# Performance work log

Measured on AMD Instinct MI355X. Metric: run time of the kernel, lower is better.

The kernel has to match this reference:

```python
import jax, jax.numpy as jnp
import numpy as np

K = 3
PAD = 1


def conv3x3(x, w, b):
    # x: [B,Ci,H,W], w: [Co,Ci,3,3] -> [B,Co,H,W]
    y = jax.lax.conv_general_dilated(
        x, w, window_strides=(1, 1), padding=((PAD, PAD), (PAD, PAD)),
        dimension_numbers=('NCHW', 'OIHW', 'NCHW'))
    return y + b[None, :, None, None]


def _gather(x_flat, idx):
    # x_flat: [C, H*W], idx: [K2*H*W] -> [C, K2*H*W]
    return x_flat[:, idx]


def deform_sample(x, off_x, off_y, mask):
    """Modulated deformable im2col (DCNv2, dg=1, stride=1, pad=1, dil=1).
    x: [B,C,H,W]; off_x, off_y, mask: [B,K2,H,W] -> cols [B,C,K2,H,W]."""
    B, C, H, W = x.shape
    K2 = K * K
    # static kernel-tap displacements relative to output pixel
    dy = jnp.repeat(jnp.arange(K), K) - PAD          # [K2]
    dx = jnp.tile(jnp.arange(K), K) - PAD            # [K2]
    gy = jnp.arange(H)[:, None].astype(x.dtype)      # [H,1]
    gx = jnp.arange(W)[None, :].astype(x.dtype)      # [1,W]
    ys = gy[None, None] + dy[None, :, None, None].astype(x.dtype) + off_y  # [B,K2,H,W]
    xs = gx[None, None] + dx[None, :, None, None].astype(x.dtype) + off_x
    y0 = jnp.floor(ys)
    x0 = jnp.floor(xs)
    wy1 = ys - y0
    wx1 = xs - x0
    xf = x.reshape(B, C, H * W)
    val = jnp.zeros((B, C, K2, H, W), x.dtype)
    for oy, ox in ((0, 0), (0, 1), (1, 0), (1, 1)):
        yy = y0 + oy
        xx = x0 + ox
        wgt = (wy1 if oy else 1.0 - wy1) * (wx1 if ox else 1.0 - wx1)
        valid = ((yy >= 0) & (yy < H) & (xx >= 0) & (xx < W)).astype(x.dtype)
        idx = (jnp.clip(yy, 0, H - 1) * W + jnp.clip(xx, 0, W - 1)).astype(jnp.int32)
        g = jax.vmap(_gather)(xf, idx.reshape(B, -1)).reshape(B, C, K2, H, W)
        val = val + (wgt * valid)[:, None] * g
    return val * mask[:, None]  # modulation, broadcast over C


def reference(x, feat, w_off, b_off, w_def, b_def):
    # offset/mask prediction conv (3*K2 channels), chunked as in the torch module
    om = conv3x3(feat, w_off, b_off)
    off_x, off_y, m = jnp.split(om, 3, axis=1)   # each [B,K2,H,W]
    mask = jax.nn.sigmoid(m)
    cols = deform_sample(x, off_x, off_y, mask)  # [B,C,K2,H,W]
    O = w_def.shape[0]
    out = jnp.einsum('bckhw,ock->bohw', cols, w_def.reshape(O, -1, K * K))
    out = out + b_def[None, :, None, None]
    return jax.nn.relu(out)


def setup_inputs() -> dict:
    key = jax.random.key(0)
    k1, k2, k3, k4 = jax.random.split(key, 4)
    B, C, O, H, W = 4, 64, 64, 128, 128
    K2 = K * K
    x = jax.random.normal(k1, (B, C, H, W), jnp.float32)
    feat = jax.random.normal(k2, (B, C, H, W), jnp.float32)
    # offset conv params: small init so offsets stay near zero (as in practice)
    w_off = jax.random.normal(k3, (3 * K2, C, 3, 3), jnp.float32) * 0.01
    b_off = jnp.zeros((3 * K2,), jnp.float32)
    w_def = jax.random.normal(k4, (O, C, 3, 3), jnp.float32) * (1.0 / np.sqrt(C * K2))
    b_def = jnp.zeros((O,), jnp.float32)
    return {"x": x, "feat": feat, "w_off": w_off, "b_off": b_off,
            "w_def": w_def, "b_def": b_def}
```

## Files before the change

### kernel.cpp

```cpp
#include <hip/hip_runtime.h>
#include <math.h>

#define Bn 4
#define Cn 64
#define On 64
#define Hn 128
#define Wn 128
#define HWn (Hn * Wn)

typedef __attribute__((ext_vector_type(8))) short s16x8;
typedef __attribute__((ext_vector_type(4))) float f32x4;

__device__ __forceinline__ unsigned short f2bf(float f) {
    unsigned u = __float_as_uint(f);
    u += 0x7fffu + ((u >> 16) & 1u);
    return (unsigned short)(u >> 16);
}
__device__ __forceinline__ float bf2f(unsigned short u) {
    return __uint_as_float(((unsigned)u) << 16);
}
__device__ __forceinline__ int swz(int row, int ch) {
    return row * 32 + (((ch ^ (row >> 1)) & 3) << 3);
}

__global__ __launch_bounds__(256) void transpose_all(const float* __restrict__ x,
                                                     const float* __restrict__ feat,
                                                     const float* __restrict__ wdef,
                                                     const float* __restrict__ woff,
                                                     ushort* __restrict__ xt,
                                                     ushort* __restrict__ ft,
                                                     ushort* __restrict__ wdT2,
                                                     ushort* __restrict__ woT2) {
    int t = threadIdx.x;
    if (blockIdx.z == 2) {
        int id = (blockIdx.y * gridDim.x + blockIdx.x) * 256 + t;
        if (id < 36864) {
            int c2 = id & 31, oc = (id >> 5) & 63, ks = id >> 11;
            int k = ks % 9, s = ks / 9;
            wdT2[id] = f2bf(wdef[(oc * 64 + s * 32 + c2) * 9 + k]);
        } else if (id < 55296) {
            int i2 = id - 36864;
            int c2 = i2 & 31, oc = (i2 >> 5) & 31, ks = i2 >> 10;
            int k = ks % 9, s = ks / 9;
            woT2[i2] = (oc < 27) ? f2bf(woff[(oc * 64 + s * 32 + c2) * 9 + k]) : (ushort)0;
        }
        return;
    }
    __shared__ float tile[64][65];
    const float* src = blockIdx.z ? feat : x;
    ushort* dst0 = blockIdx.z ? ft : xt;
    int b = blockIdx.y, hw0 = blockIdx.x * 64;
    int lane = t & 63, grp = t >> 6;
    const float* xb = src + (size_t)b * Cn * HWn;
#pragma unroll
    for (int i = 0; i < 16; ++i) {
        int c = grp * 16 + i;
        tile[lane][c] = xb[(size_t)c * HWn + hw0 + lane];
    }
    __syncthreads();
#pragma unroll
    for (int jj = 0; jj < 2; ++jj) {
        int px = jj * 32 + (t >> 3), ch = t & 7;
        s16x8 p;
#pragma unroll
        for (int j = 0; j < 8; ++j) p[j] = (short)f2bf(tile[px][ch * 8 + j]);
        *(s16x8*)(dst0 + ((size_t)(b * HWn + hw0 + px)) * Cn + ch * 8) = p;
    }
}

__global__ __launch_bounds__(256, 3) void off_conv_kernel(const ushort* __restrict__ ft,
                                                          const ushort* __restrict__ woT2,
                                                          const float* __restrict__ b_off,
                                                          float* __restrict__ om) {
    __shared__ __align__(16) char smem[43776];
    ushort* s_win = (ushort*)smem;
    ushort* s_wgt = (ushort*)(smem + 25344);
    float* s_out = (float*)smem;

    int t = threadIdx.x;
    int wv = t >> 6, l = t & 63;
    int q = l >> 4, r = l & 15;
    int h = blockIdx.x, b = blockIdx.y;
    const ushort* ft_b = ft + (size_t)b * HWn * Cn;

    f32x4 zero = {0.f, 0.f, 0.f, 0.f};
    s16x8 zz = {0, 0, 0, 0, 0, 0, 0, 0};
    f32x4 acc[2][2];
    acc[0][0] = zero; acc[0][1] = zero; acc[1][0] = zero; acc[1][1] = zero;

    for (int s = 0; s < 2; ++s) {
        for (int j = t; j < 1560; j += 256) {
            int row = j / 520, rm = j - row * 520;
            int col = rm >> 2, ch = rm & 3;
            int rs = min(max(h - 1 + row, 0), Hn - 1);
            int cs = min(max(col - 1, 0), Wn - 1);
            s16x8 v = *(const s16x8*)(ft_b + (size_t)(rs * Wn + cs) * Cn + s * 32 + ch * 8);
            *(s16x8*)&s_win[swz(row * 132 + col, ch)] = v;
        }
        for (int j = t; j < 1152; j += 256) {
            int ro = j >> 2, ch = j & 3;
            s16x8 v = *(const s16x8*)(woT2 + (size_t)s * 9216 + ro * 32 + ch * 8);
            *(s16x8*)&s_wgt[swz(ro, ch)] = v;
        }
        __syncthreads();
#pragma unroll 3
        for (int k = 0; k < 9; ++k) {
            int dy = k / 3 - 1, dx = k % 3 - 1;
            int y = h + dy;
            bool yv = (y >= 0) && (y < Hn);
#pragma unroll
            for (int mt = 0; mt < 2; ++mt) {
                int px = wv * 32 + mt * 16 + r;
                int xx = px + dx;
                bool valid = yv && (xx >= 0) && (xx < Wn);
                int lin = (dy + 1) * 132 + px + dx + 1;
                s16x8 av = *(const s16x8*)&s_win[swz(lin, q)];
                av = valid ? av : zz;
#pragma unroll
                for (int ot = 0; ot < 2; ++ot) {
                    s16x8 bv = *(const s16x8*)&s_wgt[swz(k * 32 + ot * 16 + r, q)];
                    acc[mt][ot] = __builtin_amdgcn_mfma_f32_16x16x32_bf16(av, bv, acc[mt][ot], 0, 0, 0);
                }
            }
        }
        __syncthreads();
    }
#pragma unroll
    for (int mt = 0; mt < 2; ++mt)
#pragma unroll
        for (int ot = 0; ot < 2; ++ot) {
            int oc = ot * 16 + r;
            float bo = (oc < 27) ? b_off[oc] : 0.f;
#pragma unroll
            for (int reg = 0; reg < 4; ++reg) {
                int px = wv * 32 + mt * 16 + q * 4 + reg;
                float v = acc[mt][ot][reg] + bo;
                if (oc >= 18 && oc < 27) v = 1.f / (1.f + __expf(-v));
                s_out[oc * 132 + px] = v;
            }
        }
    __syncthreads();
    for (int idx = t; idx < 27 * 128; idx += 256) {
        int o = idx >> 7, px = idx & 127;
        om[((size_t)b * 27 + o) * HWn + h * Wn + px] = s_out[o * 132 + px];
    }
}

__global__ __launch_bounds__(256, 3) void mega_kernel(const ushort* __restrict__ xt,
                                                      const ushort* __restrict__ wdT2,
                                                      const float* __restrict__ om,
                                                      const float* __restrict__ b_def,
                                                      float* __restrict__ out) {
    __shared__ __align__(16) char smem[24576];
    ushort* s_win = (ushort*)smem;
    float* s_out = (float*)smem;

    int t = threadIdx.x;
    int wv = t >> 6, l = t & 63;
    int q = l >> 4, r = l & 15;
    int blk = (blockIdx.x & 7) * 256 + (blockIdx.x >> 3);
    int p0 = blk * 32;
    int b = p0 >> 14;
    int rem = p0 & (HWn - 1);
    int h = rem >> 7;
    int wbase = rem & (Wn - 1);
    int pxh = wv & 1, och = wv >> 1;
    int pxi = pxh * 16 + r;
    float pxif = (float)pxi;
    const ushort* xt_b = xt + (size_t)b * HWn * Cn;

#pragma unroll
    for (int i = 0; i < 6; ++i) {
        int jb = i * 256 + wv * 64;
        int j = jb + l;
        int lin = j >> 3, slot = j & 7;
        int linc = min(lin, 179);
        int cidx = (slot - lin) & 7;
        int row = linc / 36, col = linc - row * 36;
        int rs = min(max(h - 2 + row, 0), Hn - 1);
        int cs = min(max(wbase - 2 + col, 0), Wn - 1);
        const ushort* gp = xt_b + (size_t)(rs * Wn + cs) * Cn + cidx * 8;
        __builtin_amdgcn_global_load_lds(
            (const __attribute__((address_space(1))) unsigned int*)gp,
            (__attribute__((address_space(3))) unsigned int*)(s_win + (size_t)jb * 8),
            16, 0, 0);
    }

    const float* om_b = om + ((size_t)b * 27) * HWn + h * Wn + wbase + pxi;
    float omv[27];
#pragma unroll
    for (int o = 0; o < 27; ++o) omv[o] = om_b[(size_t)o * HWn];

    bool okp = true;
#pragma unroll
    for (int k = 0; k < 9; ++k) {
        float uy = (float)(k / 3 - 1) + omv[9 + k];
        float ux = pxif + (float)(k % 3 - 1) + omv[k];
        okp = okp && (uy >= -2.f) && (uy < 2.f) && (ux >= -2.f) && (ux < 33.f);
    }
    int fast = __all(okp) ? 1 : 0;

    __syncthreads();

    f32x4 zero = {0.f, 0.f, 0.f, 0.f};
    f32x4 acc[2];
    acc[0] = zero; acc[1] = zero;

    if (fast) {
#pragma unroll 3
        for (int k = 0; k < 9; ++k) {
            float uy = (float)(k / 3 - 1) + omv[9 + k];
            float ux = pxif + (float)(k % 3 - 1) + omv[k];
            float mv = omv[18 + k];
            float y0f = floorf(uy), x0f = floorf(ux);
            float fy = uy - y0f, fx = ux - x0f;
            int iy = (int)y0f + 2;
            int ix = (int)x0f + 2;
            int yab = h + (int)y0f, xab = wbase + (int)x0f;
            bool vy0 = (yab >= 0) && (yab < Hn);
            bool vy1 = (yab + 1 >= 0) && (yab + 1 < Hn);
            bool vx0 = (xab >= 0) && (xab < Wn);
            bool vx1 = (xab + 1 >= 0) && (xab + 1 < Wn);
            float g0 = (vy0 && vx0) ? (1.f - fy) * (1.f - fx) * mv : 0.f;
            float g1 = (vy0 && vx1) ? (1.f - fy) * fx * mv : 0.f;
            float g2 = (vy1 && vx0) ? fy * (1.f - fx) * mv : 0.f;
            float g3 = (vy1 && vx1) ? fy * fx * mv : 0.f;
            int l0 = iy * 36 + ix, l1 = l0 + 1, l2 = l0 + 36, l3 = l0 + 37;
            s16x8 bw[2][2];
#pragma unroll
            for (int s = 0; s < 2; ++s)
#pragma unroll
                for (int ot = 0; ot < 2; ++ot)
                    bw[s][ot] = *(const s16x8*)(wdT2 + (size_t)s * 18432
                                                + (size_t)(k * 64 + och * 32 + ot * 16 + r) * 32 + q * 8);
            s16x8 af[2];
#pragma unroll
            for (int s = 0; s < 2; ++s) {
                int c = s * 4 + q;
                s16x8 q0 = *(const s16x8*)&s_win[l0 * 64 + (((c + l0) & 7) << 3)];
                s16x8 q1 = *(const s16x8*)&s_win[l1 * 64 + (((c + l1) & 7) << 3)];
                s16x8 q2 = *(const s16x8*)&s_win[l2 * 64 + (((c + l2) & 7) << 3)];
                s16x8 q3 = *(const s16x8*)&s_win[l3 * 64 + (((c + l3) & 7) << 3)];
                s16x8 p;
#pragma unroll
                for (int j = 0; j < 8; ++j) {
                    float rr = g0 * bf2f((unsigned short)q0[j]) + g1 * bf2f((unsigned short)q1[j])
                             + g2 * bf2f((unsigned short)q2[j]) + g3 * bf2f((unsigned short)q3[j]);
                    p[j] = (short)f2bf(rr);
                }
                af[s] = p;
            }
#pragma unroll
            for (int s = 0; s < 2; ++s)
#pragma unroll
                for (int ot = 0; ot < 2; ++ot)
                    acc[ot] = __builtin_amdgcn_mfma_f32_16x16x32_bf16(af[s], bw[s][ot], acc[ot], 0, 0, 0);
        }
    } else {
#pragma unroll 1
        for (int k = 0; k < 9; ++k) {
            float ys = (float)(h + k / 3 - 1) + omv[9 + k];
            float xs = (float)(wbase + pxi + k % 3 - 1) + omv[k];
            float mv = omv[18 + k];
            float y0f = floorf(ys), x0f = floorf(xs);
            float fy = ys - y0f, fx = xs - x0f;
            int y0 = (int)y0f, x0 = (int)x0f;
            float g[4];
            int a[4];
#pragma unroll
            for (int n = 0; n < 4; ++n) {
                int yy = y0 + (n >> 1), xx = x0 + (n & 1);
                bool valid = (yy >= 0) && (yy < Hn) && (xx >= 0) && (xx < Wn);
                float wgt = ((n >> 1) ? fy : 1.f - fy) * ((n & 1) ? fx : 1.f - fx) * mv;
                g[n] = valid ? wgt : 0.f;
                int yc = min(max(yy, 0), Hn - 1), xc = min(max(xx, 0), Wn - 1);
                a[n] = (yc * Wn + xc) * Cn;
            }
#pragma unroll
            for (int s = 0; s < 2; ++s) {
                int c = s * 32 + q * 8;
                s16x8 q0 = *(const s16x8*)(xt_b + a[0] + c);
                s16x8 q1 = *(const s16x8*)(xt_b + a[1] + c);
                s16x8 q2 = *(const s16x8*)(xt_b + a[2] + c);
                s16x8 q3 = *(const s16x8*)(xt_b + a[3] + c);
                s16x8 af;
#pragma unroll
                for (int j = 0; j < 8; ++j) {
                    float rr = g[0] * bf2f((unsigned short)q0[j]) + g[1] * bf2f((unsigned short)q1[j])
                             + g[2] * bf2f((unsigned short)q2[j]) + g[3] * bf2f((unsigned short)q3[j]);
                    af[j] = (short)f2bf(rr);
                }
#pragma unroll
                for (int ot = 0; ot < 2; ++ot) {
                    s16x8 bv = *(const s16x8*)(wdT2 + (size_t)s * 18432
                                               + (size_t)(k * 64 + och * 32 + ot * 16 + r) * 32 + q * 8);
                    acc[ot] = __builtin_amdgcn_mfma_f32_16x16x32_bf16(af, bv, acc[ot], 0, 0, 0);
                }
            }
        }
    }
    __syncthreads();

#pragma unroll
    for (int ot = 0; ot < 2; ++ot) {
        int oc = och * 32 + ot * 16 + r;
        float bv = b_def[oc];
        f32x4 vv;
#pragma unroll
        for (int reg = 0; reg < 4; ++reg) vv[reg] = fmaxf(acc[ot][reg] + bv, 0.f);
        *(f32x4*)&s_out[oc * 34 + pxh * 16 + q * 4] = vv;
    }
    __syncthreads();
    {
        int px = t & 31, og = t >> 5;
        float* ob = out + ((size_t)b * On) * HWn + h * Wn + wbase;
#pragma unroll
        for (int j = 0; j < 8; ++j) {
            int oc = og * 8 + j;
            ob[(size_t)oc * HWn + px] = s_out[oc * 34 + px];
        }
    }
}

extern "C" void kernel_launch(void* const* d_in, const int* in_sizes, int n_in,
                              void* d_out, int out_size, void* d_ws, size_t ws_size,
                              hipStream_t stream) {
    const float* x = (const float*)d_in[0];
    const float* feat = (const float*)d_in[1];
    const float* w_off = (const float*)d_in[2];
    const float* b_off = (const float*)d_in[3];
    const float* w_def = (const float*)d_in[4];
    const float* b_def = (const float*)d_in[5];
    float* out = (float*)d_out;

    char* ws = (char*)d_ws;
    ushort* xt = (ushort*)ws;
    ushort* ft = (ushort*)(ws + 8388608);
    ushort* wdT2 = (ushort*)(ws + 16777216);
    ushort* woT2 = (ushort*)(ws + 16850944);
    float* om = (float*)(ws + 16887808);

    hipLaunchKernelGGL(transpose_all, dim3(HWn / 64, Bn, 3), dim3(256), 0, stream,
                       x, feat, w_def, w_off, xt, ft, wdT2, woT2);
    hipLaunchKernelGGL(off_conv_kernel, dim3(Hn, Bn), dim3(256), 0, stream,
                       ft, woT2, b_off, om);
    hipLaunchKernelGGL(mega_kernel, dim3((Bn * HWn) / 32), dim3(256), 0, stream,
                       xt, wdT2, om, b_def, out);
}
```

Measured before the change: 141.0 us.

## Split offset conv per half-row and widen deform tile to 2x32 pixels

The offset-conv kernel now processes half a row (64 pixels) per block, which doubles the grid and shrinks its LDS footprint. This should raise occupancy and parallelism. The deform mega kernel now covers a 2-row by 32-pixel tile, with each wave computing all 64 output channels instead of half. This reuses the staged 5-row input window across two rows and halves the number of blocks, in exchange for more accumulator registers, more weight loads per wave, and slightly more LDS.

After: 128.3 us. 9.0% less time.

```diff
diff --git a/kernel.cpp b/kernel.cpp
--- a/kernel.cpp
+++ b/kernel.cpp
@@ -72,30 +72,31 @@
                                                           const ushort* __restrict__ woT2,
                                                           const float* __restrict__ b_off,
                                                           float* __restrict__ om) {
-    __shared__ __align__(16) char smem[43776];
+    __shared__ __align__(16) char smem[31488];
     ushort* s_win = (ushort*)smem;
-    ushort* s_wgt = (ushort*)(smem + 25344);
+    ushort* s_wgt = (ushort*)(smem + 13056);
     float* s_out = (float*)smem;
 
     int t = threadIdx.x;
     int wv = t >> 6, l = t & 63;
     int q = l >> 4, r = l & 15;
-    int h = blockIdx.x, b = blockIdx.y;
+    int h = blockIdx.x >> 1, wb = (blockIdx.x & 1) * 64;
+    int b = blockIdx.y;
     const ushort* ft_b = ft + (size_t)b * HWn * Cn;
 
     f32x4 zero = {0.f, 0.f, 0.f, 0.f};
     s16x8 zz = {0, 0, 0, 0, 0, 0, 0, 0};
-    f32x4 acc[2][2];
-    acc[0][0] = zero; acc[0][1] = zero; acc[1][0] = zero; acc[1][1] = zero;
+    f32x4 acc[2];
+    acc[0] = zero; acc[1] = zero;
 
     for (int s = 0; s < 2; ++s) {
-        for (int j = t; j < 1560; j += 256) {
-            int row = j / 520, rm = j - row * 520;
+        for (int j = t; j < 816; j += 256) {
+            int row = j / 272, rm = j - row * 272;
             int col = rm >> 2, ch = rm & 3;
             int rs = min(max(h - 1 + row, 0), Hn - 1);
-            int cs = min(max(col - 1, 0), Wn - 1);
+            int cs = min(max(wb - 1 + col, 0), Wn - 1);
             s16x8 v = *(const s16x8*)(ft_b + (size_t)(rs * Wn + cs) * Cn + s * 32 + ch * 8);
-            *(s16x8*)&s_win[swz(row * 132 + col, ch)] = v;
+            *(s16x8*)&s_win[swz(row * 68 + col, ch)] = v;
         }
         for (int j = t; j < 1152; j += 256) {
             int ro = j >> 2, ch = j & 3;
@@ -108,41 +109,36 @@
             int dy = k / 3 - 1, dx = k % 3 - 1;
             int y = h + dy;
             bool yv = (y >= 0) && (y < Hn);
-#pragma unroll
-            for (int mt = 0; mt < 2; ++mt) {
-                int px = wv * 32 + mt * 16 + r;
-                int xx = px + dx;
-                bool valid = yv && (xx >= 0) && (xx < Wn);
-                int lin = (dy + 1) * 132 + px + dx + 1;
-                s16x8 av = *(const s16x8*)&s_win[swz(lin, q)];
-                av = valid ? av : zz;
-#pragma unroll
-                for (int ot = 0; ot < 2; ++ot) {
-                    s16x8 bv = *(const s16x8*)&s_wgt[swz(k * 32 + ot * 16 + r, q)];
-                    acc[mt][ot] = __builtin_amdgcn_mfma_f32_16x16x32_bf16(av, bv, acc[mt][ot], 0, 0, 0);
-                }
+            int px = wv * 16 + r;
+            int xx = wb + px + dx;
+            bool valid = yv && (xx >= 0) && (xx < Wn);
+            int lin = (dy + 1) * 68 + px + dx + 1;
+            s16x8 av = *(const s16x8*)&s_win[swz(lin, q)];
+            av = valid ? av : zz;
+#pragma unroll
+            for (int ot = 0; ot < 2; ++ot) {
+                s16x8 bv = *(const s16x8*)&s_wgt[swz(k * 32 + ot * 16 + r, q)];
+                acc[ot] = __builtin_amdgcn_mfma_f32_16x16x32_bf16(av, bv, acc[ot], 0, 0, 0);
             }
         }
         __syncthreads();
     }
 #pragma unroll
-    for (int mt = 0; mt < 2; ++mt)
-#pragma unroll
-        for (int ot = 0; ot < 2; ++ot) {
-            int oc = ot * 16 + r;
-            float bo = (oc < 27) ? b_off[oc] : 0.f;
-#pragma unroll
-            for (int reg = 0; reg < 4; ++reg) {
-                int px = wv * 32 + mt * 16 + q * 4 + reg;
-                float v = acc[mt][ot][reg] + bo;
-                if (oc >= 18 && oc < 27) v = 1.f / (1.f + __expf(-v));
-                s_out[oc * 132 + px] = v;
-            }
-        }
-    __syncthreads();
-    for (int idx = t; idx < 27 * 128; idx += 256) {
-        int o = idx >> 7, px = idx & 127;
-        om[((size_t)b * 27 + o) * HWn + h * Wn + px] = s_out[o * 132 + px];
+    for (int ot = 0; ot < 2; ++ot) {
+        int oc = ot * 16 + r;
+        float bo = (oc < 27) ? b_off[oc] : 0.f;
+#pragma unroll
+        for (int reg = 0; reg < 4; ++reg) {
+            int px = wv * 16 + q * 4 + reg;
+            float v = acc[ot][reg] + bo;
+            if (oc >= 18 && oc < 27) v = 1.f / (1.f + __expf(-v));
+            s_out[oc * 68 + px] = v;
+        }
+    }
+    __syncthreads();
+    for (int idx = t; idx < 27 * 64; idx += 256) {
+        int o = idx >> 6, px = idx & 63;
+        om[((size_t)b * 27 + o) * HWn + h * Wn + wb + px] = s_out[o * 68 + px];
     }
 }
 
@@ -151,30 +147,31 @@
                                                       const float* __restrict__ om,
                                                       const float* __restrict__ b_def,
                                                       float* __restrict__ out) {
-    __shared__ __align__(16) char smem[24576];
+    __shared__ __align__(16) char smem[28672];
     ushort* s_win = (ushort*)smem;
     float* s_out = (float*)smem;
 
     int t = threadIdx.x;
     int wv = t >> 6, l = t & 63;
     int q = l >> 4, r = l & 15;
-    int blk = (blockIdx.x & 7) * 256 + (blockIdx.x >> 3);
-    int p0 = blk * 32;
-    int b = p0 >> 14;
-    int rem = p0 & (HWn - 1);
-    int h = rem >> 7;
-    int wbase = rem & (Wn - 1);
-    int pxh = wv & 1, och = wv >> 1;
+    int blk = (blockIdx.x & 7) * 128 + (blockIdx.x >> 3);
+    int b = blk >> 8;
+    int gi = blk & 255;
+    int h = (gi >> 2) << 1;
+    int wbase = (gi & 3) << 5;
+    int rowoff = wv >> 1, pxh = wv & 1;
+    int hrow = h + rowoff;
     int pxi = pxh * 16 + r;
     float pxif = (float)pxi;
+    float rowofff = (float)rowoff;
     const ushort* xt_b = xt + (size_t)b * HWn * Cn;
 
 #pragma unroll
-    for (int i = 0; i < 6; ++i) {
+    for (int i = 0; i < 7; ++i) {
         int jb = i * 256 + wv * 64;
         int j = jb + l;
         int lin = j >> 3, slot = j & 7;
-        int linc = min(lin, 179);
+        int linc = min(lin, 215);
         int cidx = (slot - lin) & 7;
         int row = linc / 36, col = linc - row * 36;
         int rs = min(max(h - 2 + row, 0), Hn - 1);
@@ -186,7 +183,7 @@
             16, 0, 0);
     }
 
-    const float* om_b = om + ((size_t)b * 27) * HWn + h * Wn + wbase + pxi;
+    const float* om_b = om + ((size_t)b * 27) * HWn + hrow * Wn + wbase + pxi;
     float omv[27];
 #pragma unroll
     for (int o = 0; o < 27; ++o) omv[o] = om_b[(size_t)o * HWn];
@@ -196,15 +193,16 @@
     for (int k = 0; k < 9; ++k) {
         float uy = (float)(k / 3 - 1) + omv[9 + k];
         float ux = pxif + (float)(k % 3 - 1) + omv[k];
-        okp = okp && (uy >= -2.f) && (uy < 2.f) && (ux >= -2.f) && (ux < 33.f);
+        okp = okp && (uy >= -2.f - rowofff) && (uy < 3.f - rowofff)
+                  && (ux >= -2.f) && (ux < 33.f);
     }
     int fast = __all(okp) ? 1 : 0;
 
     __syncthreads();
 
     f32x4 zero = {0.f, 0.f, 0.f, 0.f};
-    f32x4 acc[2];
-    acc[0] = zero; acc[1] = zero;
+    f32x4 acc[4];
+    acc[0] = zero; acc[1] = zero; acc[2] = zero; acc[3] = zero;
 
     if (fast) {
 #pragma unroll 3
@@ -214,9 +212,9 @@
             float mv = omv[18 + k];
             float y0f = floorf(uy), x0f = floorf(ux);
             float fy = uy - y0f, fx = ux - x0f;
-            int iy = (int)y0f + 2;
+            int iy = (int)y0f + 2 + rowoff;
             int ix = (int)x0f + 2;
-            int yab = h + (int)y0f, xab = wbase + (int)x0f;
+            int yab = hrow + (int)y0f, xab = wbase + (int)x0f;
             bool vy0 = (yab >= 0) && (yab < Hn);
             bool vy1 = (yab + 1 >= 0) && (yab + 1 < Hn);
             bool vx0 = (xab >= 0) && (xab < Wn);
@@ -226,13 +224,13 @@
             float g2 = (vy1 && vx0) ? fy * (1.f - fx) * mv : 0.f;
             float g3 = (vy1 && vx1) ? fy * fx * mv : 0.f;
             int l0 = iy * 36 + ix, l1 = l0 + 1, l2 = l0 + 36, l3 = l0 + 37;
-            s16x8 bw[2][2];
+            s16x8 bw[2][4];
 #pragma unroll
             for (int s = 0; s < 2; ++s)
 #pragma unroll
-                for (int ot = 0; ot < 2; ++ot)
+                for (int ot = 0; ot < 4; ++ot)
                     bw[s][ot] = *(const s16x8*)(wdT2 + (size_t)s * 18432
-                                                + (size_t)(k * 64 + och * 32 + ot * 16 + r) * 32 + q * 8);
+                                                + (size_t)(k * 64 + ot * 16 + r) * 32 + q * 8);
             s16x8 af[2];
 #pragma unroll
             for (int s = 0; s < 2; ++s) {
@@ -253,13 +251,13 @@
 #pragma unroll
             for (int s = 0; s < 2; ++s)
 #pragma unroll
-                for (int ot = 0; ot < 2; ++ot)
+                for (int ot = 0; ot < 4; ++ot)
                     acc[ot] = __builtin_amdgcn_mfma_f32_16x16x32_bf16(af[s], bw[s][ot], acc[ot], 0, 0, 0);
         }
     } else {
 #pragma unroll 1
         for (int k = 0; k < 9; ++k) {
-            float ys = (float)(h + k / 3 - 1) + omv[9 + k];
+            float ys = (float)(hrow + k / 3 - 1) + omv[9 + k];
             float xs = (float)(wbase + pxi + k % 3 - 1) + omv[k];
             float mv = omv[18 + k];
             float y0f = floorf(ys), x0f = floorf(xs);
@@ -291,9 +289,9 @@
                     af[j] = (short)f2bf(rr);
                 }
 #pragma unroll
-                for (int ot = 0; ot < 2; ++ot) {
+                for (int ot = 0; ot < 4; ++ot) {
                     s16x8 bv = *(const s16x8*)(wdT2 + (size_t)s * 18432
-                                               + (size_t)(k * 64 + och * 32 + ot * 16 + r) * 32 + q * 8);
+                                               + (size_t)(k * 64 + ot * 16 + r) * 32 + q * 8);
                     acc[ot] = __builtin_amdgcn_mfma_f32_16x16x32_bf16(af, bv, acc[ot], 0, 0, 0);
                 }
             }
@@ -302,22 +300,23 @@
     __syncthreads();
 
 #pragma unroll
-    for (int ot = 0; ot < 2; ++ot) {
-        int oc = och * 32 + ot * 16 + r;
+    for (int ot = 0; ot < 4; ++ot) {
+        int oc = ot * 16 + r;
         float bv = b_def[oc];
         f32x4 vv;
 #pragma unroll
         for (int reg = 0; reg < 4; ++reg) vv[reg] = fmaxf(acc[ot][reg] + bv, 0.f);
-        *(f32x4*)&s_out[oc * 34 + pxh * 16 + q * 4] = vv;
+        *(f32x4*)&s_out[oc * 68 + rowoff * 32 + pxh * 16 + q * 4] = vv;
     }
     __syncthreads();
     {
-        int px = t & 31, og = t >> 5;
-        float* ob = out + ((size_t)b * On) * HWn + h * Wn + wbase;
-#pragma unroll
-        for (int j = 0; j < 8; ++j) {
-            int oc = og * 8 + j;
-            ob[(size_t)oc * HWn + px] = s_out[oc * 34 + px];
+        int px = t & 63, og = t >> 6;
+        int rg = h + (px >> 5);
+        float* ob = out + ((size_t)b * On) * HWn + rg * Wn + wbase + (px & 31);
+#pragma unroll
+        for (int j = 0; j < 16; ++j) {
+            int oc = og * 16 + j;
+            ob[(size_t)oc * HWn] = s_out[oc * 68 + px];
         }
     }
 }
@@ -342,8 +341,8 @@
 
     hipLaunchKernelGGL(transpose_all, dim3(HWn / 64, Bn, 3), dim3(256), 0, stream,
                        x, feat, w_def, w_off, xt, ft, wdT2, woT2);
-    hipLaunchKernelGGL(off_conv_kernel, dim3(Hn, Bn), dim3(256), 0, stream,
+    hipLaunchKernelGGL(off_conv_kernel, dim3(Hn * 2, Bn), dim3(256), 0, stream,
                        ft, woT2, b_off, om);
-    hipLaunchKernelGGL(mega_kernel, dim3((Bn * HWn) / 32), dim3(256), 0, stream,
+    hipLaunchKernelGGL(mega_kernel, dim3((Bn * HWn) / 64), dim3(256), 0, stream,
                        xt, wdT2, om, b_def, out);
 }
```
